# Kernel tuning notes

Hardware: AMD Instinct MI355X
Metric: run time of the kernel (lower is better)

The kernel has to match this reference:

```python
import jax, jax.numpy as jnp
import numpy as np

HEADS = 16
DIM_HEAD = 64
SCALE = DIM_HEAD ** -0.5


def setup_inputs() -> dict:
    key = jax.random.key(0)
    k1, k2, k3, k4 = jax.random.split(key, 4)
    dim = 1024
    inner = HEADS * DIM_HEAD  # 1024
    b, n = 4, 2048
    x = jax.random.normal(k1, (b, n, dim), dtype=jnp.float32)
    # weights stored as [in, out] (equivalent math to torch Linear)
    w_qkv = jax.random.normal(k2, (dim, inner * 3), dtype=jnp.float32) * (dim ** -0.5)
    w_out = jax.random.normal(k3, (inner, dim), dtype=jnp.float32) * (inner ** -0.5)
    b_out = jax.random.normal(k4, (dim,), dtype=jnp.float32) * 0.01
    return {"x": x, "w_qkv": w_qkv, "w_out": w_out, "b_out": b_out}


def reference(x, w_qkv, w_out, b_out):
    b, n, dim = x.shape
    qkv = x @ w_qkv                                   # [b, n, 3*inner]
    q, k, v = jnp.split(qkv, 3, axis=-1)
    def to_heads(t):
        return t.reshape(b, n, HEADS, DIM_HEAD).transpose(0, 2, 1, 3)  # b h n d
    q, k, v = to_heads(q) * SCALE, to_heads(k), to_heads(v)
    dots = jnp.einsum('bhid,bhjd->bhij', q, k)        # [b, h, n, n]
    mask_value = -jnp.finfo(dots.dtype).max
    causal_mask = jnp.triu(jnp.ones((n, n), dtype=bool), k=1)
    dots = jnp.where(causal_mask, mask_value, dots)
    attn = jax.nn.softmax(dots, axis=-1)
    out = jnp.einsum('bhij,bhjd->bhid', attn, v)      # [b, h, n, d]
    out = out.transpose(0, 2, 1, 3).reshape(b, n, HEADS * DIM_HEAD)
    return out @ w_out + b_out
```

## Files before the change

### kernel.cpp

```cpp
#include <hip/hip_runtime.h>
#include <hip/hip_bf16.h>
#include <stdint.h>

typedef __attribute__((ext_vector_type(8))) short bf16x8;
typedef __attribute__((ext_vector_type(4))) float f32x4;
typedef __attribute__((ext_vector_type(4))) unsigned int uint32x4;

#define TOKENS 8192
#define DMODEL 1024
#define NQKV   3072
#define NSEQ   2048
#define NHEAD  16
#define DHEAD  64

__device__ __forceinline__ ushort f32_bf16(float f) {
    uint32_t u = __builtin_bit_cast(uint32_t, f);
    u = (u + 0x7fffu + ((u >> 16) & 1u)) >> 16;
    return (ushort)u;
}

__device__ __forceinline__ unsigned int cvt_pk_bf16(float lo, float hi) {
    unsigned int r;
    asm("v_cvt_pk_bf16_f32 %0, %1, %2" : "=v"(r) : "v"(lo), "v"(hi));
    return r;
}
__device__ __forceinline__ void permlane32_swap(unsigned int& a, unsigned int& b) {
    asm("v_permlane32_swap_b32 %0, %1" : "+v"(a), "+v"(b));
}
__device__ __forceinline__ void permlane16_swap(unsigned int& a, unsigned int& b) {
    asm("v_permlane16_swap_b32 %0, %1" : "+v"(a), "+v"(b));
}

__device__ __forceinline__ void gload16(const void* g, void* l) {
    __builtin_amdgcn_global_load_lds(
        (const __attribute__((address_space(1))) void*)g,
        (__attribute__((address_space(3))) void*)l, 16, 0, 0);
}

__global__ void cvt_x_kernel(const float* __restrict__ x, ushort* __restrict__ xb) {
    int i = blockIdx.x * 256 + threadIdx.x;
    float4 v = reinterpret_cast<const float4*>(x)[i];
    ushort4 o;
    o.x = f32_bf16(v.x); o.y = f32_bf16(v.y);
    o.z = f32_bf16(v.z); o.w = f32_bf16(v.w);
    reinterpret_cast<ushort4*>(xb)[i] = o;
}

__global__ __launch_bounds__(256) void cvt_wt_kernel(
    const float* __restrict__ w, ushort* __restrict__ wt, int N)
{
    __shared__ float tile[64][65];
    const int tid = threadIdx.x;
    const int r  = tid >> 4;
    const int c4 = (tid & 15) * 4;
    const int n0 = blockIdx.x * 64;
    const int k0 = blockIdx.y * 64;
    #pragma unroll
    for (int i = 0; i < 4; ++i) {
        const float4 v = *reinterpret_cast<const float4*>(&w[(size_t)(k0 + r + i * 16) * N + n0 + c4]);
        tile[r + i * 16][c4 + 0] = v.x;
        tile[r + i * 16][c4 + 1] = v.y;
        tile[r + i * 16][c4 + 2] = v.z;
        tile[r + i * 16][c4 + 3] = v.w;
    }
    __syncthreads();
    #pragma unroll
    for (int i = 0; i < 4; ++i) {
        ushort4 o;
        o.x = f32_bf16(tile[c4 + 0][r + i * 16]);
        o.y = f32_bf16(tile[c4 + 1][r + i * 16]);
        o.z = f32_bf16(tile[c4 + 2][r + i * 16]);
        o.w = f32_bf16(tile[c4 + 3][r + i * 16]);
        *reinterpret_cast<ushort4*>(&wt[(size_t)(n0 + r + i * 16) * 1024 + k0 + c4]) = o;
    }
}

template<int MODE>
__global__ __launch_bounds__(256) void gemm_bt(
    const ushort* __restrict__ A, const ushort* __restrict__ Bt,
    ushort* __restrict__ Qb, ushort* __restrict__ Kb, ushort* __restrict__ Vtb,
    float* __restrict__ Out, const float* __restrict__ bias)
{
    constexpr int K = 1024;
    __shared__ __align__(16) ushort As[128 * 32];
    __shared__ __align__(16) ushort Bs[128 * 32];

    const int lane = threadIdx.x & 63;
    const int w    = threadIdx.x >> 6;
    const int l16  = lane & 15;
    const int g    = lane >> 4;
    const int row0 = blockIdx.y * 128;
    const int col0 = blockIdx.x * 128;
    const int wr   = (w >> 1) * 64;
    const int wc   = (w & 1) * 64;

    const int srow = w * 16 + (lane >> 2);
    const int scol = (lane & 3) * 8;
    const ushort* Ag = A  + (size_t)(row0 + srow) * K + scol;
    const ushort* Bg = Bt + (size_t)(col0 + srow) * K + scol;
    ushort* AsW = As + w * (16 * 32);
    ushort* BsW = Bs + w * (16 * 32);

    f32x4 acc[4][4] = {};

    for (int kk = 0; kk < K; kk += 32) {
        gload16(Ag + kk,          AsW);
        gload16(Ag + 64 * K + kk, AsW + 64 * 32);
        gload16(Bg + kk,          BsW);
        gload16(Bg + 64 * K + kk, BsW + 64 * 32);
        __syncthreads();
        bf16x8 a[4], b[4];
        #pragma unroll
        for (int m = 0; m < 4; ++m)
            a[m] = *reinterpret_cast<const bf16x8*>(&As[(wr + m * 16 + l16) * 32 + 8 * g]);
        #pragma unroll
        for (int n = 0; n < 4; ++n)
            b[n] = *reinterpret_cast<const bf16x8*>(&Bs[(wc + n * 16 + l16) * 32 + 8 * g]);
        #pragma unroll
        for (int m = 0; m < 4; ++m)
            #pragma unroll
            for (int n = 0; n < 4; ++n)
                acc[m][n] = __builtin_amdgcn_mfma_f32_16x16x32_bf16(a[m], b[n], acc[m][n], 0, 0, 0);
        __syncthreads();
    }

    if (MODE == 0) {
        const int part = col0 >> 10;
        const float QSC = 0.18033688011112042f;
        #pragma unroll
        for (int m = 0; m < 4; ++m) {
            const int trow = row0 + wr + m * 16 + 4 * g;
            #pragma unroll
            for (int n = 0; n < 4; ++n) {
                const int c  = col0 + wc + n * 16 + l16;
                const int cc = c & 1023;
                const int h  = cc >> 6, d = cc & 63;
                #pragma unroll
                for (int jj = 0; jj < 4; ++jj) {
                    const int t  = trow + jj;
                    const int bb = t >> 11, nn = t & 2047;
                    const float v = acc[m][n][jj];
                    const size_t bhid = (size_t)(bb * NHEAD + h);
                    if (part == 0)
                        Qb[(bhid * NSEQ + nn) * DHEAD + d] = f32_bf16(v * QSC);
                    else if (part == 1)
                        Kb[(bhid * NSEQ + nn) * DHEAD + d] = f32_bf16(v);
                    else
                        Vtb[bhid * (NSEQ * DHEAD) + (size_t)(nn >> 5) * (DHEAD * 32)
                            + d * 32 + (nn & 31)] = f32_bf16(v);
                }
            }
        }
    } else {
        #pragma unroll
        for (int m = 0; m < 4; ++m) {
            const int trow = row0 + wr + m * 16 + 4 * g;
            #pragma unroll
            for (int n = 0; n < 4; ++n) {
                const int c = col0 + wc + n * 16 + l16;
                const float bv = bias[c];
                #pragma unroll
                for (int jj = 0; jj < 4; ++jj)
                    Out[(size_t)(trow + jj) * DMODEL + c] = acc[m][n][jj] + bv;
            }
        }
    }
}

__device__ __forceinline__ void attn_qk(
    int kt, int qr0s, int l16, int g,
    const bf16x8 (&kk)[4][2],
    const bf16x8 qf0, const bf16x8 qf1,
    f32x4 (&oacc)[4], float& mrun, float& lsum,
    bf16x8& pf0, bf16x8& pf1)
{
    const f32x4 zero = {};
    f32x4 s[4];
    #pragma unroll
    for (int t = 0; t < 4; ++t) {
        s[t] = __builtin_amdgcn_mfma_f32_16x16x32_bf16(kk[t][0], qf0, zero, 0, 0, 0);
        s[t] = __builtin_amdgcn_mfma_f32_16x16x32_bf16(kk[t][1], qf1, s[t], 0, 0, 0);
    }
    if (kt + 63 > qr0s) {
        const int kb = kt + 4 * g - (qr0s + l16);
        #pragma unroll
        for (int t = 0; t < 4; ++t)
            #pragma unroll
            for (int jj = 0; jj < 4; ++jj)
                if (kb + 16 * t + jj > 0) s[t][jj] = -1e30f;
    }
    float mx = fmaxf(fmaxf(s[0][0], s[0][1]), fmaxf(s[0][2], s[0][3]));
    #pragma unroll
    for (int t = 1; t < 4; ++t)
        mx = fmaxf(mx, fmaxf(fmaxf(s[t][0], s[t][1]), fmaxf(s[t][2], s[t][3])));
    mx = fmaxf(mx, __shfl_xor(mx, 16));
    mx = fmaxf(mx, __shfl_xor(mx, 32));
    const float mn = fmaxf(mrun, mx);
    const float sc = __builtin_amdgcn_exp2f(mrun - mn);
    mrun = mn;
    float ps = 0.f;
    unsigned int pw[4][2];
    #pragma unroll
    for (int t = 0; t < 4; ++t) {
        const float p0 = __builtin_amdgcn_exp2f(s[t][0] - mn);
        const float p1 = __builtin_amdgcn_exp2f(s[t][1] - mn);
        const float p2 = __builtin_amdgcn_exp2f(s[t][2] - mn);
        const float p3 = __builtin_amdgcn_exp2f(s[t][3] - mn);
        ps += (p0 + p1) + (p2 + p3);
        pw[t][0] = cvt_pk_bf16(p0, p1);
        pw[t][1] = cvt_pk_bf16(p2, p3);
    }
    ps += __shfl_xor(ps, 16);
    ps += __shfl_xor(ps, 32);
    lsum = lsum * sc + ps;
    unsigned int a0 = pw[0][0], a1 = pw[0][1], b0 = pw[1][0], b1 = pw[1][1];
    permlane32_swap(a0, b0); permlane32_swap(a1, b1);
    permlane16_swap(a0, b0); permlane16_swap(a1, b1);
    pf0 = __builtin_bit_cast(bf16x8, (uint32x4){a0, a1, b0, b1});
    unsigned int c0 = pw[2][0], c1 = pw[2][1], d0 = pw[3][0], d1 = pw[3][1];
    permlane32_swap(c0, d0); permlane32_swap(c1, d1);
    permlane16_swap(c0, d0); permlane16_swap(c1, d1);
    pf1 = __builtin_bit_cast(bf16x8, (uint32x4){c0, c1, d0, d1});
    float scj[4];
    #pragma unroll
    for (int jj = 0; jj < 4; ++jj) scj[jj] = __shfl(sc, 4 * g + jj);
    #pragma unroll
    for (int dt = 0; dt < 4; ++dt)
        #pragma unroll
        for (int jj = 0; jj < 4; ++jj) oacc[dt][jj] *= scj[jj];
}

__global__ __launch_bounds__(256) void attn_kernel(
    const ushort* __restrict__ Qb, const ushort* __restrict__ Kb,
    const ushort* __restrict__ Vt, ushort* __restrict__ Ob)
{
    __shared__ __align__(16) ushort Klds[2][4096];
    __shared__ __align__(16) ushort Vlds[2][4096];

    const int lane = threadIdx.x & 63;
    const int w    = threadIdx.x >> 6;
    const int l16  = lane & 15;
    const int g    = lane >> 4;

    const int bid = blockIdx.x;
    const int xcd = bid & 7, ii = bid >> 3;
    const int bh  = xcd * 8 + (ii >> 4);
    const int jlo = ii & 15;
    const int jhi = 31 - jlo;

    const int qr0_lo = jlo * 64 + w * 16;
    const int qr0_hi = jhi * 64 + w * 16;
    const int nt = jhi + 1;

    const ushort* QpL = Qb + ((size_t)bh * NSEQ + qr0_lo + l16) * DHEAD + 8 * g;
    const ushort* QpH = Qb + ((size_t)bh * NSEQ + qr0_hi + l16) * DHEAD + 8 * g;
    const bf16x8 qfL0 = *reinterpret_cast<const bf16x8*>(QpL);
    const bf16x8 qfL1 = *reinterpret_cast<const bf16x8*>(QpL + 32);
    const bf16x8 qfH0 = *reinterpret_cast<const bf16x8*>(QpH);
    const bf16x8 qfH1 = *reinterpret_cast<const bf16x8*>(QpH + 32);

    const ushort* Kg = Kb + (size_t)bh * (NSEQ * DHEAD);
    const ushort* Vg = Vt + (size_t)bh * (NSEQ * DHEAD);

    const int q0   = w * 2;
    const int krow0 = (q0 & 3) * 16 + (lane >> 2);
    const int kcol0 = (lane & 3) * 8;

    f32x4 oaccL[4] = {}, oaccH[4] = {};
    float mrunL = -1e30f, lsumL = 0.f, mrunH = -1e30f, lsumH = 0.f;

    {
        const int kt = 0;
        #pragma unroll
        for (int i = 0; i < 2; ++i) {
            const int q = q0 + i;
            const int row = krow0 + i * 16;
            const int h = q >> 2;
            gload16(Kg + (size_t)(kt + ((q & 3) * 16 + (lane >> 2))) * 64 + h * 32 + kcol0,
                    &Klds[0][q * 512]);
            gload16(Vg + (size_t)kt * 64 + q * 512 + lane * 8,
                    &Vlds[0][q * 512]);
            (void)row;
        }
    }
    __syncthreads();

    for (int t = 0; t < nt; ++t) {
        const int cur = t & 1;
        if (t + 1 < nt) {
            const int kt1 = (t + 1) * 64;
            #pragma unroll
            for (int i = 0; i < 2; ++i) {
                const int q = q0 + i;
                const int h = q >> 2;
                gload16(Kg + (size_t)(kt1 + ((q & 3) * 16 + (lane >> 2))) * 64 + h * 32 + kcol0,
                        &Klds[cur ^ 1][q * 512]);
                gload16(Vg + (size_t)kt1 * 64 + q * 512 + lane * 8,
                        &Vlds[cur ^ 1][q * 512]);
            }
        }
        const int kt = t * 64;
        bf16x8 kk[4][2];
        #pragma unroll
        for (int tt = 0; tt < 4; ++tt) {
            #pragma unroll
            for (int h = 0; h < 2; ++h)
                kk[tt][h] = *reinterpret_cast<const bf16x8*>(
                    &Klds[cur][h * 2048 + (16 * tt + l16) * 32 + 8 * g]);
        }
        bf16x8 pfH0, pfH1, pfL0, pfL1;
        attn_qk(kt, qr0_hi, l16, g, kk, qfH0, qfH1, oaccH, mrunH, lsumH, pfH0, pfH1);
        const bool doLo = (t <= jlo);
        if (doLo)
            attn_qk(kt, qr0_lo, l16, g, kk, qfL0, qfL1, oaccL, mrunL, lsumL, pfL0, pfL1);
        #pragma unroll
        for (int dt = 0; dt < 4; ++dt) {
            const bf16x8 v0 = *reinterpret_cast<const bf16x8*>(
                &Vlds[cur][(dt * 16 + l16) * 32 + 8 * g]);
            const bf16x8 v1 = *reinterpret_cast<const bf16x8*>(
                &Vlds[cur][2048 + (dt * 16 + l16) * 32 + 8 * g]);
            oaccH[dt] = __builtin_amdgcn_mfma_f32_16x16x32_bf16(pfH0, v0, oaccH[dt], 0, 0, 0);
            oaccH[dt] = __builtin_amdgcn_mfma_f32_16x16x32_bf16(pfH1, v1, oaccH[dt], 0, 0, 0);
            if (doLo) {
                oaccL[dt] = __builtin_amdgcn_mfma_f32_16x16x32_bf16(pfL0, v0, oaccL[dt], 0, 0, 0);
                oaccL[dt] = __builtin_amdgcn_mfma_f32_16x16x32_bf16(pfL1, v1, oaccL[dt], 0, 0, 0);
            }
        }
        __syncthreads();
    }

    const int bb = bh >> 4, h = bh & 15;
    {
        const float inv = 1.0f / lsumH;
        float invj[4];
        #pragma unroll
        for (int jj = 0; jj < 4; ++jj) invj[jj] = __shfl(inv, 4 * g + jj);
        #pragma unroll
        for (int jj = 0; jj < 4; ++jj) {
            const size_t t = (size_t)bb * NSEQ + qr0_hi + 4 * g + jj;
            #pragma unroll
            for (int dt = 0; dt < 4; ++dt)
                Ob[t * DMODEL + h * DHEAD + dt * 16 + l16] = f32_bf16(oaccH[dt][jj] * invj[jj]);
        }
    }
    {
        const float inv = 1.0f / lsumL;
        float invj[4];
        #pragma unroll
        for (int jj = 0; jj < 4; ++jj) invj[jj] = __shfl(inv, 4 * g + jj);
        #pragma unroll
        for (int jj = 0; jj < 4; ++jj) {
            const size_t t = (size_t)bb * NSEQ + qr0_lo + 4 * g + jj;
            #pragma unroll
            for (int dt = 0; dt < 4; ++dt)
                Ob[t * DMODEL + h * DHEAD + dt * 16 + l16] = f32_bf16(oaccL[dt][jj] * invj[jj]);
        }
    }
}

extern "C" void kernel_launch(void* const* d_in, const int* in_sizes, int n_in,
                              void* d_out, int out_size, void* d_ws, size_t ws_size,
                              hipStream_t stream)
{
    const float* x     = (const float*)d_in[0];
    const float* w_qkv = (const float*)d_in[1];
    const float* w_out = (const float*)d_in[2];
    const float* b_out = (const float*)d_in[3];
    float* out = (float*)d_out;

    char* ws = (char*)d_ws;
    ushort* x_bf   = (ushort*)(ws);
    ushort* wqkv_t = (ushort*)(ws + 16777216);
    ushort* wout_t = (ushort*)(ws + 23068672);
    ushort* q_bf   = (ushort*)(ws + 25165824);
    ushort* k_bf   = (ushort*)(ws + 41943040);
    ushort* vt_bf  = (ushort*)(ws + 58720256);
    ushort* attn_bf = x_bf;

    cvt_x_kernel<<<dim3(TOKENS * DMODEL / 4 / 256), dim3(256), 0, stream>>>(x, x_bf);
    cvt_wt_kernel<<<dim3(NQKV / 64, 1024 / 64), dim3(256), 0, stream>>>(w_qkv, wqkv_t, NQKV);
    cvt_wt_kernel<<<dim3(1024 / 64, 1024 / 64), dim3(256), 0, stream>>>(w_out, wout_t, 1024);

    gemm_bt<0><<<dim3(NQKV / 128, TOKENS / 128), dim3(256), 0, stream>>>(
        x_bf, wqkv_t, q_bf, k_bf, vt_bf, nullptr, nullptr);

    attn_kernel<<<dim3(1024), dim3(256), 0, stream>>>(q_bf, k_bf, vt_bf, attn_bf);

    gemm_bt<1><<<dim3(DMODEL / 128, TOKENS / 128), dim3(256), 0, stream>>>(
        attn_bf, wout_t, nullptr, nullptr, nullptr, out, b_out);
}
```

Before: 224.7 us.

## Use lazy softmax rescaling and permlane-based row reductions in attention

The online softmax now rescales the running output and denominator only when a new row max exceeds the stored max by more than a threshold (wave-uniform via __any). Otherwise the old max is kept as the exponent reference, which skips the shuffles and 16 multiplies per step. The row max and sum reductions across lane groups now use permlane16/32 swaps instead of __shfl_xor, and the max tree is flattened into 3-input max ops. The risk is larger exponent values, bounded by the threshold, and a divergent branch.

```diff
diff --git a/kernel.cpp b/kernel.cpp
--- a/kernel.cpp
+++ b/kernel.cpp
@@ -29,6 +29,32 @@
 }
 __device__ __forceinline__ void permlane16_swap(unsigned int& a, unsigned int& b) {
     asm("v_permlane16_swap_b32 %0, %1" : "+v"(a), "+v"(b));
+}
+__device__ __forceinline__ unsigned opaque_copy(unsigned x) {
+    unsigned y;
+    asm("v_mov_b32 %0, %1" : "=v"(y) : "v"(x));
+    return y;
+}
+
+__device__ __forceinline__ float red_max_g(float x) {
+    unsigned a = __builtin_bit_cast(unsigned, x);
+    unsigned b = opaque_copy(a);
+    permlane16_swap(a, b);
+    float r = fmaxf(__builtin_bit_cast(float, a), __builtin_bit_cast(float, b));
+    unsigned c = __builtin_bit_cast(unsigned, r);
+    unsigned d = opaque_copy(c);
+    permlane32_swap(c, d);
+    return fmaxf(__builtin_bit_cast(float, c), __builtin_bit_cast(float, d));
+}
+__device__ __forceinline__ float red_sum_g(float x) {
+    unsigned a = __builtin_bit_cast(unsigned, x);
+    unsigned b = opaque_copy(a);
+    permlane16_swap(a, b);
+    float r = __builtin_bit_cast(float, a) + __builtin_bit_cast(float, b);
+    unsigned c = __builtin_bit_cast(unsigned, r);
+    unsigned d = opaque_copy(c);
+    permlane32_swap(c, d);
+    return __builtin_bit_cast(float, c) + __builtin_bit_cast(float, d);
 }
 
 __device__ __forceinline__ void gload16(const void* g, void* l) {
@@ -189,30 +215,40 @@
             for (int jj = 0; jj < 4; ++jj)
                 if (kb + 16 * t + jj > 0) s[t][jj] = -1e30f;
     }
-    float mx = fmaxf(fmaxf(s[0][0], s[0][1]), fmaxf(s[0][2], s[0][3]));
-    #pragma unroll
-    for (int t = 1; t < 4; ++t)
-        mx = fmaxf(mx, fmaxf(fmaxf(s[t][0], s[t][1]), fmaxf(s[t][2], s[t][3])));
-    mx = fmaxf(mx, __shfl_xor(mx, 16));
-    mx = fmaxf(mx, __shfl_xor(mx, 32));
-    const float mn = fmaxf(mrun, mx);
-    const float sc = __builtin_amdgcn_exp2f(mrun - mn);
-    mrun = mn;
+    const float m0 = fmaxf(fmaxf(s[0][0], s[0][1]), s[0][2]);
+    const float m1 = fmaxf(fmaxf(s[0][3], s[1][0]), s[1][1]);
+    const float m2 = fmaxf(fmaxf(s[1][2], s[1][3]), s[2][0]);
+    const float m3 = fmaxf(fmaxf(s[2][1], s[2][2]), s[2][3]);
+    const float m4 = fmaxf(fmaxf(s[3][0], s[3][1]), s[3][2]);
+    const float m5 = fmaxf(fmaxf(m0, m1), m2);
+    const float m6 = fmaxf(fmaxf(m3, m4), s[3][3]);
+    float mx = red_max_g(fmaxf(m5, m6));
+    if (__any(mx > mrun + 8.0f)) {
+        const float mn = fmaxf(mrun, mx);
+        const float sc = __builtin_amdgcn_exp2f(mrun - mn);
+        mrun = mn;
+        lsum *= sc;
+        float scj[4];
+        #pragma unroll
+        for (int jj = 0; jj < 4; ++jj) scj[jj] = __shfl(sc, 4 * g + jj);
+        #pragma unroll
+        for (int dt = 0; dt < 4; ++dt)
+            #pragma unroll
+            for (int jj = 0; jj < 4; ++jj) oacc[dt][jj] *= scj[jj];
+    }
     float ps = 0.f;
     unsigned int pw[4][2];
     #pragma unroll
     for (int t = 0; t < 4; ++t) {
-        const float p0 = __builtin_amdgcn_exp2f(s[t][0] - mn);
-        const float p1 = __builtin_amdgcn_exp2f(s[t][1] - mn);
-        const float p2 = __builtin_amdgcn_exp2f(s[t][2] - mn);
-        const float p3 = __builtin_amdgcn_exp2f(s[t][3] - mn);
+        const float p0 = __builtin_amdgcn_exp2f(s[t][0] - mrun);
+        const float p1 = __builtin_amdgcn_exp2f(s[t][1] - mrun);
+        const float p2 = __builtin_amdgcn_exp2f(s[t][2] - mrun);
+        const float p3 = __builtin_amdgcn_exp2f(s[t][3] - mrun);
         ps += (p0 + p1) + (p2 + p3);
         pw[t][0] = cvt_pk_bf16(p0, p1);
         pw[t][1] = cvt_pk_bf16(p2, p3);
     }
-    ps += __shfl_xor(ps, 16);
-    ps += __shfl_xor(ps, 32);
-    lsum = lsum * sc + ps;
+    lsum += red_sum_g(ps);
     unsigned int a0 = pw[0][0], a1 = pw[0][1], b0 = pw[1][0], b1 = pw[1][1];
     permlane32_swap(a0, b0); permlane32_swap(a1, b1);
     permlane16_swap(a0, b0); permlane16_swap(a1, b1);
@@ -221,13 +257,6 @@
     permlane32_swap(c0, d0); permlane32_swap(c1, d1);
     permlane16_swap(c0, d0); permlane16_swap(c1, d1);
     pf1 = __builtin_bit_cast(bf16x8, (uint32x4){c0, c1, d0, d1});
-    float scj[4];
-    #pragma unroll
-    for (int jj = 0; jj < 4; ++jj) scj[jj] = __shfl(sc, 4 * g + jj);
-    #pragma unroll
-    for (int dt = 0; dt < 4; ++dt)
-        #pragma unroll
-        for (int jj = 0; jj < 4; ++jj) oacc[dt][jj] *= scj[jj];
 }
 
 __global__ __launch_bounds__(256) void attn_kernel(
@@ -263,24 +292,20 @@
     const ushort* Vg = Vt + (size_t)bh * (NSEQ * DHEAD);
 
     const int q0   = w * 2;
-    const int krow0 = (q0 & 3) * 16 + (lane >> 2);
     const int kcol0 = (lane & 3) * 8;
 
     f32x4 oaccL[4] = {}, oaccH[4] = {};
     float mrunL = -1e30f, lsumL = 0.f, mrunH = -1e30f, lsumH = 0.f;
 
     {
-        const int kt = 0;
         #pragma unroll
         for (int i = 0; i < 2; ++i) {
             const int q = q0 + i;
-            const int row = krow0 + i * 16;
             const int h = q >> 2;
-            gload16(Kg + (size_t)(kt + ((q & 3) * 16 + (lane >> 2))) * 64 + h * 32 + kcol0,
+            gload16(Kg + (size_t)((q & 3) * 16 + (lane >> 2)) * 64 + h * 32 + kcol0,
                     &Klds[0][q * 512]);
-            gload16(Vg + (size_t)kt * 64 + q * 512 + lane * 8,
+            gload16(Vg + (size_t)q * 512 + lane * 8,
                     &Vlds[0][q * 512]);
-            (void)row;
         }
     }
     __syncthreads();
```

Result: faster. 215.9 us (-3.9%).
